# Performance work log

Measured on AMD Instinct MI355X. Metric: run time of the kernel, lower is better.

The kernel has to match this reference:

```python
import jax, jax.numpy as jnp
import numpy as np

N_NODES = 100000
N_EDGES = 1600000
H_FEATS = 64


def setup_inputs() -> dict:
    key = jax.random.key(0)
    k_h, k_src, k_dst, k_w1, k_b1, k_w2, k_b2 = jax.random.split(key, 7)
    h = jax.random.normal(k_h, (N_NODES, H_FEATS), dtype=jnp.float32)
    src = jax.random.randint(k_src, (N_EDGES,), 0, N_NODES, dtype=jnp.int64)
    dst = jax.random.randint(k_dst, (N_EDGES,), 0, N_NODES, dtype=jnp.int64)
    # Linear params (torch Linear: y = x @ W.T + b). Store as [in, out] for jnp.
    lim1 = 1.0 / np.sqrt(2 * H_FEATS)
    W1 = jax.random.uniform(k_w1, (2 * H_FEATS, H_FEATS), minval=-lim1, maxval=lim1, dtype=jnp.float32)
    b1 = jax.random.uniform(k_b1, (H_FEATS,), minval=-lim1, maxval=lim1, dtype=jnp.float32)
    lim2 = 1.0 / np.sqrt(H_FEATS)
    W2 = jax.random.uniform(k_w2, (H_FEATS, 1), minval=-lim2, maxval=lim2, dtype=jnp.float32)
    b2 = jax.random.uniform(k_b2, (1,), minval=-lim2, maxval=lim2, dtype=jnp.float32)
    return {"h": h, "src": src, "dst": dst, "W1": W1, "b1": b1, "W2": W2, "b2": b2}


def reference(h, src, dst, W1, b1, W2, b2):
    # Gather src/dst node features per edge, avoid materializing the concat by
    # splitting W1 into the src-half and dst-half of the contraction.
    W1s, W1d = W1[:H_FEATS], W1[H_FEATS:]            # each [h, h]
    h_src = h[src]                                    # [E, h]
    h_dst = h[dst]                                    # [E, h]
    hidden = jax.nn.relu(h_src @ W1s + h_dst @ W1d + b1)  # [E, h]
    score = (hidden @ W2 + b2)[:, 0]                  # [E]
    return score
```

## Files before the change

kernel.cpp:

```cpp
#include <hip/hip_runtime.h>
#include <hip/hip_fp16.h>


#define HF   64
#define PADH 136

typedef __attribute__((ext_vector_type(8))) short bf16x8;
typedef __attribute__((ext_vector_type(4))) float f32x4;

__device__ __forceinline__ short f2bf(float x) {
    unsigned u = __builtin_bit_cast(unsigned, x);
    unsigned r = (u + 0x7fffu + ((u >> 16) & 1u)) >> 16;
    return (short)r;
}

__global__ __launch_bounds__(256) void node_proj_kernel(
    const float* __restrict__ h, const float* __restrict__ W1,
    const float* __restrict__ b1, __half* __restrict__ P,
    __half* __restrict__ Q, int n_nodes)
{
    __shared__ __half eb[64 * PADH];

    const int tid  = threadIdx.x;
    const int wave = tid >> 6;
    const int lane = tid & 63;
    const int q    = lane >> 4;
    const int n    = lane & 15;

    const int n0   = blockIdx.x * 64;
    const int nrow = (n_nodes - n0 < 64) ? (n_nodes - n0) : 64;

    int arow = n0 + wave * 16 + n;
    if (arow >= n_nodes) arow = n_nodes - 1;
    const float* hr = h + (size_t)arow * HF + q * 8;
    const float4 u0 = *(const float4*)(hr);
    const float4 u1 = *(const float4*)(hr + 4);
    const float4 v0 = *(const float4*)(hr + 32);
    const float4 v1 = *(const float4*)(hr + 36);

    bf16x8 bfrag[8][2];
    #pragma unroll
    for (int t = 0; t < 8; ++t) {
        const float* wb = W1 + ((t >= 4) ? HF * HF : 0) + (t & 3) * 16 + n;
        #pragma unroll
        for (int kb = 0; kb < 2; ++kb) {
            #pragma unroll
            for (int j = 0; j < 8; ++j)
                bfrag[t][kb][j] = f2bf(wb[(kb * 32 + q * 8 + j) * HF]);
        }
    }
    const float bias_t[4] = { b1[0 * 16 + n], b1[1 * 16 + n],
                              b1[2 * 16 + n], b1[3 * 16 + n] };

    bf16x8 a0, a1;
    a0[0]=f2bf(u0.x); a0[1]=f2bf(u0.y); a0[2]=f2bf(u0.z); a0[3]=f2bf(u0.w);
    a0[4]=f2bf(u1.x); a0[5]=f2bf(u1.y); a0[6]=f2bf(u1.z); a0[7]=f2bf(u1.w);
    a1[0]=f2bf(v0.x); a1[1]=f2bf(v0.y); a1[2]=f2bf(v0.z); a1[3]=f2bf(v0.w);
    a1[4]=f2bf(v1.x); a1[5]=f2bf(v1.y); a1[6]=f2bf(v1.z); a1[7]=f2bf(v1.w);

    f32x4 acc[8];
    #pragma unroll
    for (int t = 0; t < 8; ++t) {
        acc[t] = (f32x4){0.f, 0.f, 0.f, 0.f};
        acc[t] = __builtin_amdgcn_mfma_f32_16x16x32_bf16(a0, bfrag[t][0], acc[t], 0, 0, 0);
        acc[t] = __builtin_amdgcn_mfma_f32_16x16x32_bf16(a1, bfrag[t][1], acc[t], 0, 0, 0);
    }

    #pragma unroll
    for (int t = 0; t < 8; ++t) {
        const float bb = (t < 4) ? bias_t[t] : 0.0f;
        #pragma unroll
        for (int r = 0; r < 4; ++r) {
            const int row = wave * 16 + q * 4 + r;
            eb[row * PADH + t * 16 + n] = __float2half(acc[t][r] + bb);
        }
    }
    __syncthreads();

    #pragma unroll
    for (int s = 0; s < 4; ++s) {
        const int idx  = tid + s * 256;
        const int row  = idx >> 4;
        const int part = idx & 15;
        if (row < nrow) {
            const uint4 v = *(const uint4*)&eb[row * PADH + part * 8];
            __half* dstp = (part < 8)
                ? (P + (size_t)(n0 + row) * HF + part * 8)
                : (Q + (size_t)(n0 + row) * HF + (part - 8) * 8);
            *(uint4*)dstp = v;
        }
    }
}

__device__ __forceinline__ float dot8_relu(uint4 pv, uint4 qv, float4 wa, float4 wb) {
    const __half2* ph = (const __half2*)&pv;
    const __half2* qh = (const __half2*)&qv;
    const float2 p0 = __half22float2(ph[0]), q0 = __half22float2(qh[0]);
    const float2 p1 = __half22float2(ph[1]), q1 = __half22float2(qh[1]);
    const float2 p2 = __half22float2(ph[2]), q2 = __half22float2(qh[2]);
    const float2 p3 = __half22float2(ph[3]), q3 = __half22float2(qh[3]);
    float acc = 0.f;
    acc = fmaf(fmaxf(p0.x + q0.x, 0.f), wa.x, acc);
    acc = fmaf(fmaxf(p0.y + q0.y, 0.f), wa.y, acc);
    acc = fmaf(fmaxf(p1.x + q1.x, 0.f), wa.z, acc);
    acc = fmaf(fmaxf(p1.y + q1.y, 0.f), wa.w, acc);
    acc = fmaf(fmaxf(p2.x + q2.x, 0.f), wb.x, acc);
    acc = fmaf(fmaxf(p2.y + q2.y, 0.f), wb.y, acc);
    acc = fmaf(fmaxf(p3.x + q3.x, 0.f), wb.z, acc);
    acc = fmaf(fmaxf(p3.y + q3.y, 0.f), wb.w, acc);
    return acc;
}

__device__ __forceinline__ float red8(float v) {
    v += __shfl_xor(v, 4, 8);
    v += __shfl_xor(v, 2, 8);
    v += __shfl_xor(v, 1, 8);
    return v;
}

__global__ __launch_bounds__(256) void edge_score_kernel(
    const __half* __restrict__ P, const __half* __restrict__ Q,
    const int* __restrict__ src, const int* __restrict__ dst,
    const float* __restrict__ W2, const float* __restrict__ b2,
    float* __restrict__ out, int n_edges)
{
    const int tid   = blockIdx.x * 256 + threadIdx.x;
    const int sub   = threadIdx.x & 7;
    const int group = tid >> 3;
    const int j0    = sub * 8;
    const int e0    = group * 8;
    if (e0 >= n_edges) return;

    const float4 w2a = *(const float4*)(W2 + j0);
    const float4 w2b = *(const float4*)(W2 + j0 + 4);
    const float bias2 = b2[0];

    if (e0 + 8 <= n_edges) {
        const int4 sA = *(const int4*)(src + e0);
        const int4 sB = *(const int4*)(src + e0 + 4);
        const int4 dA = *(const int4*)(dst + e0);
        const int4 dB = *(const int4*)(dst + e0 + 4);

        const uint4 p0 = *(const uint4*)(P + (size_t)sA.x * HF + j0);
        const uint4 p1 = *(const uint4*)(P + (size_t)sA.y * HF + j0);
        const uint4 p2 = *(const uint4*)(P + (size_t)sA.z * HF + j0);
        const uint4 p3 = *(const uint4*)(P + (size_t)sA.w * HF + j0);
        const uint4 p4 = *(const uint4*)(P + (size_t)sB.x * HF + j0);
        const uint4 p5 = *(const uint4*)(P + (size_t)sB.y * HF + j0);
        const uint4 p6 = *(const uint4*)(P + (size_t)sB.z * HF + j0);
        const uint4 p7 = *(const uint4*)(P + (size_t)sB.w * HF + j0);
        const uint4 q0 = *(const uint4*)(Q + (size_t)dA.x * HF + j0);
        const uint4 q1 = *(const uint4*)(Q + (size_t)dA.y * HF + j0);
        const uint4 q2 = *(const uint4*)(Q + (size_t)dA.z * HF + j0);
        const uint4 q3 = *(const uint4*)(Q + (size_t)dA.w * HF + j0);
        const uint4 q4 = *(const uint4*)(Q + (size_t)dB.x * HF + j0);
        const uint4 q5 = *(const uint4*)(Q + (size_t)dB.y * HF + j0);
        const uint4 q6 = *(const uint4*)(Q + (size_t)dB.z * HF + j0);
        const uint4 q7 = *(const uint4*)(Q + (size_t)dB.w * HF + j0);

        float s0 = red8(dot8_relu(p0, q0, w2a, w2b));
        float s1 = red8(dot8_relu(p1, q1, w2a, w2b));
        float s2 = red8(dot8_relu(p2, q2, w2a, w2b));
        float s3 = red8(dot8_relu(p3, q3, w2a, w2b));
        float s4 = red8(dot8_relu(p4, q4, w2a, w2b));
        float s5 = red8(dot8_relu(p5, q5, w2a, w2b));
        float s6 = red8(dot8_relu(p6, q6, w2a, w2b));
        float s7 = red8(dot8_relu(p7, q7, w2a, w2b));

        if (sub == 0) {
            *(float4*)(out + e0)     = make_float4(s0 + bias2, s1 + bias2,
                                                   s2 + bias2, s3 + bias2);
            *(float4*)(out + e0 + 4) = make_float4(s4 + bias2, s5 + bias2,
                                                   s6 + bias2, s7 + bias2);
        }
    } else {
        for (int e = e0; e < n_edges; ++e) {
            const int s = src[e];
            const int d = dst[e];
            const uint4 pv = *(const uint4*)(P + (size_t)s * HF + j0);
            const uint4 qv = *(const uint4*)(Q + (size_t)d * HF + j0);
            float sc = red8(dot8_relu(pv, qv, w2a, w2b));
            if (sub == 0) out[e] = sc + bias2;
        }
    }
}

extern "C" void kernel_launch(void* const* d_in, const int* in_sizes, int n_in,
                              void* d_out, int out_size, void* d_ws, size_t ws_size,
                              hipStream_t stream) {
    const float* h   = (const float*)d_in[0];
    const int*   src = (const int*)d_in[1];
    const int*   dst = (const int*)d_in[2];
    const float* W1  = (const float*)d_in[3];
    const float* b1  = (const float*)d_in[4];
    const float* W2  = (const float*)d_in[5];
    const float* b2  = (const float*)d_in[6];
    float* out = (float*)d_out;

    const int n_nodes = in_sizes[0] / HF;
    const int n_edges = in_sizes[1];

    __half* P = (__half*)d_ws;
    __half* Q = P + (size_t)n_nodes * HF;

    const int nblocks1 = (n_nodes + 63) / 64;
    node_proj_kernel<<<nblocks1, 256, 0, stream>>>(h, W1, b1, P, Q, n_nodes);

    const int ngroups  = (n_edges + 7) / 8;
    const int nblocks2 = (ngroups + 31) / 32;
    edge_score_kernel<<<nblocks2, 256, 0, stream>>>(P, Q, src, dst, W2, b2, out, n_edges);
}
```

Baseline: 149.1 us.

## Stage W1 via LDS with coalesced loads and process two node tiles per block

```diff
diff --git a/kernel.cpp b/kernel.cpp
--- a/kernel.cpp
+++ b/kernel.cpp
@@ -4,14 +4,15 @@
 
 #define HF   64
 #define PADH 136
+#define TPB  2
 
 typedef __attribute__((ext_vector_type(8))) short bf16x8;
 typedef __attribute__((ext_vector_type(4))) float f32x4;
 
-__device__ __forceinline__ short f2bf(float x) {
+__device__ __forceinline__ unsigned short f2bf(float x) {
     unsigned u = __builtin_bit_cast(unsigned, x);
     unsigned r = (u + 0x7fffu + ((u >> 16) & 1u)) >> 16;
-    return (short)r;
+    return (unsigned short)r;
 }
 
 __global__ __launch_bounds__(256) void node_proj_kernel(
@@ -19,7 +20,9 @@
     const float* __restrict__ b1, __half* __restrict__ P,
     __half* __restrict__ Q, int n_nodes)
 {
-    __shared__ __half eb[64 * PADH];
+    __shared__ __align__(16) char smem[64 * PADH * 2];
+    unsigned short* wt = (unsigned short*)smem;
+    __half*         eb = (__half*)smem;
 
     const int tid  = threadIdx.x;
     const int wave = tid >> 6;
@@ -27,67 +30,91 @@
     const int q    = lane >> 4;
     const int n    = lane & 15;
 
-    const int n0   = blockIdx.x * 64;
-    const int nrow = (n_nodes - n0 < 64) ? (n_nodes - n0) : 64;
-
-    int arow = n0 + wave * 16 + n;
-    if (arow >= n_nodes) arow = n_nodes - 1;
-    const float* hr = h + (size_t)arow * HF + q * 8;
-    const float4 u0 = *(const float4*)(hr);
-    const float4 u1 = *(const float4*)(hr + 4);
-    const float4 v0 = *(const float4*)(hr + 32);
-    const float4 v1 = *(const float4*)(hr + 36);
+    #pragma unroll
+    for (int it = 0; it < 8; ++it) {
+        const int idx = tid + it * 256;
+        const float4 v = *(const float4*)(W1 + idx * 4);
+        const int r  = idx >> 4;
+        const int k  = r & 63;
+        const int cb = ((idx & 15) * 4) + ((r >= 64) ? 64 : 0);
+        const unsigned short bv[4] = { f2bf(v.x), f2bf(v.y), f2bf(v.z), f2bf(v.w) };
+        #pragma unroll
+        for (int i = 0; i < 4; ++i) {
+            const int c = cb + i;
+            const int chunk = (k >> 3) ^ (c & 7);
+            wt[c * 64 + chunk * 8 + (k & 7)] = bv[i];
+        }
+    }
+    __syncthreads();
 
     bf16x8 bfrag[8][2];
     #pragma unroll
     for (int t = 0; t < 8; ++t) {
-        const float* wb = W1 + ((t >= 4) ? HF * HF : 0) + (t & 3) * 16 + n;
+        const int c = t * 16 + n;
         #pragma unroll
         for (int kb = 0; kb < 2; ++kb) {
-            #pragma unroll
-            for (int j = 0; j < 8; ++j)
-                bfrag[t][kb][j] = f2bf(wb[(kb * 32 + q * 8 + j) * HF]);
+            const int phys = (kb * 4 + q) ^ (n & 7);
+            bfrag[t][kb] = *(const bf16x8*)&wt[c * 64 + phys * 8];
         }
     }
     const float bias_t[4] = { b1[0 * 16 + n], b1[1 * 16 + n],
                               b1[2 * 16 + n], b1[3 * 16 + n] };
-
-    bf16x8 a0, a1;
-    a0[0]=f2bf(u0.x); a0[1]=f2bf(u0.y); a0[2]=f2bf(u0.z); a0[3]=f2bf(u0.w);
-    a0[4]=f2bf(u1.x); a0[5]=f2bf(u1.y); a0[6]=f2bf(u1.z); a0[7]=f2bf(u1.w);
-    a1[0]=f2bf(v0.x); a1[1]=f2bf(v0.y); a1[2]=f2bf(v0.z); a1[3]=f2bf(v0.w);
-    a1[4]=f2bf(v1.x); a1[5]=f2bf(v1.y); a1[6]=f2bf(v1.z); a1[7]=f2bf(v1.w);
-
-    f32x4 acc[8];
+    __syncthreads();
+
     #pragma unroll
-    for (int t = 0; t < 8; ++t) {
-        acc[t] = (f32x4){0.f, 0.f, 0.f, 0.f};
-        acc[t] = __builtin_amdgcn_mfma_f32_16x16x32_bf16(a0, bfrag[t][0], acc[t], 0, 0, 0);
-        acc[t] = __builtin_amdgcn_mfma_f32_16x16x32_bf16(a1, bfrag[t][1], acc[t], 0, 0, 0);
-    }
-
-    #pragma unroll
-    for (int t = 0; t < 8; ++t) {
-        const float bb = (t < 4) ? bias_t[t] : 0.0f;
-        #pragma unroll
-        for (int r = 0; r < 4; ++r) {
-            const int row = wave * 16 + q * 4 + r;
-            eb[row * PADH + t * 16 + n] = __float2half(acc[t][r] + bb);
-        }
-    }
-    __syncthreads();
-
-    #pragma unroll
-    for (int s = 0; s < 4; ++s) {
-        const int idx  = tid + s * 256;
-        const int row  = idx >> 4;
-        const int part = idx & 15;
-        if (row < nrow) {
-            const uint4 v = *(const uint4*)&eb[row * PADH + part * 8];
-            __half* dstp = (part < 8)
-                ? (P + (size_t)(n0 + row) * HF + part * 8)
-                : (Q + (size_t)(n0 + row) * HF + (part - 8) * 8);
-            *(uint4*)dstp = v;
+    for (int it = 0; it < TPB; ++it) {
+        const int n0 = (blockIdx.x * TPB + it) * 64;
+        if (n0 >= n_nodes) break;
+        const int nrow = (n_nodes - n0 < 64) ? (n_nodes - n0) : 64;
+
+        bf16x8 a0, a1;
+        {
+            int row = n0 + wave * 16 + n;
+            if (row >= n_nodes) row = n_nodes - 1;
+            const float* hr = h + (size_t)row * HF + q * 8;
+            const float4 u0 = *(const float4*)(hr);
+            const float4 u1 = *(const float4*)(hr + 4);
+            const float4 v0 = *(const float4*)(hr + 32);
+            const float4 v1 = *(const float4*)(hr + 36);
+            a0[0]=f2bf(u0.x); a0[1]=f2bf(u0.y); a0[2]=f2bf(u0.z); a0[3]=f2bf(u0.w);
+            a0[4]=f2bf(u1.x); a0[5]=f2bf(u1.y); a0[6]=f2bf(u1.z); a0[7]=f2bf(u1.w);
+            a1[0]=f2bf(v0.x); a1[1]=f2bf(v0.y); a1[2]=f2bf(v0.z); a1[3]=f2bf(v0.w);
+            a1[4]=f2bf(v1.x); a1[5]=f2bf(v1.y); a1[6]=f2bf(v1.z); a1[7]=f2bf(v1.w);
+        }
+
+        f32x4 acc[8];
+        #pragma unroll
+        for (int t = 0; t < 8; ++t) {
+            acc[t] = (f32x4){0.f, 0.f, 0.f, 0.f};
+            acc[t] = __builtin_amdgcn_mfma_f32_16x16x32_bf16(a0, bfrag[t][0], acc[t], 0, 0, 0);
+            acc[t] = __builtin_amdgcn_mfma_f32_16x16x32_bf16(a1, bfrag[t][1], acc[t], 0, 0, 0);
+        }
+
+        if (it > 0) __syncthreads();
+
+        #pragma unroll
+        for (int t = 0; t < 8; ++t) {
+            const float bb = (t < 4) ? bias_t[t] : 0.0f;
+            #pragma unroll
+            for (int r = 0; r < 4; ++r) {
+                const int row = wave * 16 + q * 4 + r;
+                eb[row * PADH + t * 16 + n] = __float2half(acc[t][r] + bb);
+            }
+        }
+        __syncthreads();
+
+        #pragma unroll
+        for (int s = 0; s < 4; ++s) {
+            const int idx  = tid + s * 256;
+            const int row  = idx >> 4;
+            const int part = idx & 15;
+            if (row < nrow) {
+                const uint4 v = *(const uint4*)&eb[row * PADH + part * 8];
+                __half* dstp = (part < 8)
+                    ? (P + (size_t)(n0 + row) * HF + part * 8)
+                    : (Q + (size_t)(n0 + row) * HF + (part - 8) * 8);
+                *(uint4*)dstp = v;
+            }
         }
     }
 }
@@ -203,7 +230,8 @@
     __half* P = (__half*)d_ws;
     __half* Q = P + (size_t)n_nodes * HF;
 
-    const int nblocks1 = (n_nodes + 63) / 64;
+    const int ntiles   = (n_nodes + 63) / 64;
+    const int nblocks1 = (ntiles + TPB - 1) / TPB;
     node_proj_kernel<<<nblocks1, 256, 0, stream>>>(h, W1, b1, P, Q, n_nodes);
 
     const int ngroups  = (n_edges + 7) / 8;
```

New measurement: 146.5 us. About the same (-1.7%).
